# Kernel optimization log

Hardware: AMD Instinct MI355X
Metric: run time of the kernel (lower is better)

## Reference

```python
import jax, jax.numpy as jnp
import numpy as np
import math

HIDDEN = 1024
HEADS = 16
HEAD_DIM = HIDDEN // HEADS
B, S = 2, 2048


def _xavier(key, shape):
    fan_in, fan_out = shape[1], shape[0]
    limit = math.sqrt(6.0 / (fan_in + fan_out))
    return jax.random.uniform(key, shape, jnp.float32, -limit, limit)


def setup_inputs() -> dict:
    key = jax.random.key(0)
    ks = jax.random.split(key, 5)
    x = jax.random.normal(ks[0], (B, S, HIDDEN), jnp.float32)
    # torch Linear stores weight as [out, in]; y = x @ W.T + b
    Wq = _xavier(ks[1], (HIDDEN, HIDDEN))
    Wk = _xavier(ks[2], (HIDDEN, HIDDEN))
    Wv = _xavier(ks[3], (HIDDEN, HIDDEN))
    Wo = _xavier(ks[4], (HIDDEN, HIDDEN))
    bq = jnp.zeros((HIDDEN,), jnp.float32)
    bk = jnp.zeros((HIDDEN,), jnp.float32)
    bv = jnp.zeros((HIDDEN,), jnp.float32)
    bo = jnp.zeros((HIDDEN,), jnp.float32)
    return {"x": x, "Wq": Wq, "bq": bq, "Wk": Wk, "bk": bk,
            "Wv": Wv, "bv": bv, "Wo": Wo, "bo": bo}


def reference(x, Wq, bq, Wk, bk, Wv, bv, Wo, bo):
    b, s, d = x.shape
    h, hd = HEADS, HEAD_DIM
    q = (x @ Wq.T + bq).reshape(b, s, h, hd).transpose(0, 2, 1, 3)  # [b,h,s,hd]
    k = (x @ Wk.T + bk).reshape(b, s, h, hd).transpose(0, 2, 1, 3)
    v = (x @ Wv.T + bv).reshape(b, s, h, hd).transpose(0, 2, 1, 3)
    scores = jnp.einsum('bhqd,bhkd->bhqk', q, k) / math.sqrt(hd)
    causal = jnp.tril(jnp.ones((s, s), bool))
    scores = jnp.where(causal, scores, -jnp.inf)
    attn = jax.nn.softmax(scores, axis=-1)
    out = jnp.einsum('bhqk,bhkd->bhqd', attn, v)  # [b,h,s,hd]
    out = out.transpose(0, 2, 1, 3).reshape(b, s, d)
    return out @ Wo.T + bo
```

## Files before the change

### kernel.cpp

```cpp
#include <hip/hip_runtime.h>
#include <hip/hip_bf16.h>


typedef __hip_bfloat16 bf16;
typedef __attribute__((ext_vector_type(8))) short short8;
typedef __attribute__((ext_vector_type(4))) short short4v;
typedef __attribute__((ext_vector_type(4))) float f32x4;

#define MFMA16(a, b, c) __builtin_amdgcn_mfma_f32_16x16x32_bf16((a), (b), (c), 0, 0, 0)

__device__ __forceinline__ void load_lds16(const void* g, void* l) {
  __builtin_amdgcn_global_load_lds(
      (const __attribute__((address_space(1))) void*)g,
      (__attribute__((address_space(3))) void*)l, 16, 0, 0);
}

#define QSCALE 0.18033688f

__global__ __launch_bounds__(256) void cvt_kernel(
    const float* __restrict__ x, const float* __restrict__ wq,
    const float* __restrict__ wk, const float* __restrict__ wv,
    const float* __restrict__ wo, bf16* __restrict__ xb,
    bf16* __restrict__ wcat) {
  const int bx = blockIdx.x;
  const float* src;
  bf16* dst;
  int ib;
  if (bx < 4096) { src = x; dst = xb; ib = bx; }
  else {
    const int wseg = (bx - 4096) >> 10;
    ib = (bx - 4096) & 1023;
    src = wseg == 0 ? wq : wseg == 1 ? wk : wseg == 2 ? wv : wo;
    dst = wcat + (size_t)wseg * 1048576;
  }
  const int i = (ib * 256 + threadIdx.x) * 4;
  const float4 v = *(const float4*)(src + i);
  short4v p;
  *(__hip_bfloat162*)&p = __float22bfloat162_rn(float2{v.x, v.y});
  *((__hip_bfloat162*)&p + 1) = __float22bfloat162_rn(float2{v.z, v.w});
  *(short4v*)(dst + i) = p;
}

__global__ __launch_bounds__(256) void qkv_kernel(
    const bf16* __restrict__ x, const bf16* __restrict__ Wcat,
    const float* __restrict__ bq, const float* __restrict__ bk,
    const float* __restrict__ bv, bf16* __restrict__ Qb,
    bf16* __restrict__ Kb, bf16* __restrict__ Vtg) {
  constexpr int K = 1024;
  __shared__ bf16 As[128 * 64];
  __shared__ bf16 Bs[128 * 64];
  const int t = threadIdx.x;
  const int lane = t & 63, w = t >> 6;
  const int quad = lane >> 4, r = lane & 15;
  const int m0 = blockIdx.y * 128;
  const int ncol = blockIdx.x * 128;
  const int seg = ncol >> 10;
  const int n0 = ncol & 1023;
  const int wm = w >> 1, wn = w & 1;

  f32x4 acc[4][4] = {};

  for (int k0 = 0; k0 < K; k0 += 64) {
    __syncthreads();
#pragma unroll
    for (int p = 0; p < 4; ++p) {
      const int c = p * 256 + w * 64 + lane;
      const int row = c >> 3;
      const int scb = (c & 7) ^ (row & 7);
      load_lds16(x + (size_t)(m0 + row) * K + k0 + scb * 8, As + c * 8);
    }
#pragma unroll
    for (int p = 0; p < 4; ++p) {
      const int c = p * 256 + w * 64 + lane;
      const int row = c >> 3;
      const int scb = (c & 7) ^ (row & 7);
      load_lds16(Wcat + (size_t)(ncol + row) * K + k0 + scb * 8, Bs + c * 8);
    }
    __syncthreads();
    short8 af[4][2], bfr[4][2];
#pragma unroll
    for (int ks = 0; ks < 2; ++ks) {
#pragma unroll
      for (int i = 0; i < 4; ++i) {
        const int ra = wm * 64 + i * 16 + r;
        af[i][ks] = *(const short8*)(As + ra * 64 +
                                     (((ks * 4 + quad) ^ (ra & 7)) * 8));
        const int rb = wn * 64 + i * 16 + r;
        bfr[i][ks] = *(const short8*)(Bs + rb * 64 +
                                      (((ks * 4 + quad) ^ (rb & 7)) * 8));
      }
    }
#pragma unroll
    for (int ks = 0; ks < 2; ++ks)
#pragma unroll
      for (int i = 0; i < 4; ++i)
#pragma unroll
        for (int j = 0; j < 4; ++j)
          acc[i][j] = MFMA16(af[i][ks], bfr[j][ks], acc[i][j]);
  }

  const float* bias = seg == 0 ? bq : seg == 1 ? bk : bv;
  const float scale = seg == 0 ? QSCALE : 1.0f;
  bf16* dst01 = seg == 0 ? Qb : Kb;
#pragma unroll
  for (int i = 0; i < 4; ++i) {
    const int m = m0 + wm * 64 + i * 16 + quad * 4;
#pragma unroll
    for (int j = 0; j < 4; ++j) {
      const int nn = n0 + wn * 64 + j * 16 + r;
      const float bv_ = bias[nn];
      if (seg == 2) {
        short4v pk;
        *(__hip_bfloat162*)&pk = __float22bfloat162_rn(
            float2{acc[i][j][0] + bv_, acc[i][j][1] + bv_});
        *((__hip_bfloat162*)&pk + 1) = __float22bfloat162_rn(
            float2{acc[i][j][2] + bv_, acc[i][j][3] + bv_});
        *(short4v*)(Vtg + (size_t)nn * 4096 + m) = pk;
      } else {
#pragma unroll
        for (int g = 0; g < 4; ++g)
          dst01[(size_t)(m + g) * 1024 + nn] =
              __float2bfloat16((acc[i][j][g] + bv_) * scale);
      }
    }
  }
}

__global__ __launch_bounds__(256) void proj_kernel(const bf16* __restrict__ X,
                                                   const bf16* __restrict__ W,
                                                   const float* __restrict__ bias,
                                                   float* __restrict__ Y) {
  constexpr int K = 1024, N = 1024;
  __shared__ bf16 As[64 * 64];
  __shared__ bf16 Bs[128 * 64];
  const int t = threadIdx.x;
  const int lane = t & 63, w = t >> 6;
  const int quad = lane >> 4, r = lane & 15;
  const int m0 = blockIdx.y * 64, n0 = blockIdx.x * 128;
  const int wm = w >> 1, wn = w & 1;

  f32x4 acc[2][4] = {};

  for (int k0 = 0; k0 < K; k0 += 64) {
    __syncthreads();
#pragma unroll
    for (int p = 0; p < 2; ++p) {
      const int c = p * 256 + w * 64 + lane;
      const int row = c >> 3;
      const int scb = (c & 7) ^ (row & 7);
      load_lds16(X + (size_t)(m0 + row) * K + k0 + scb * 8, As + c * 8);
    }
#pragma unroll
    for (int p = 0; p < 4; ++p) {
      const int c = p * 256 + w * 64 + lane;
      const int row = c >> 3;
      const int scb = (c & 7) ^ (row & 7);
      load_lds16(W + (size_t)(n0 + row) * K + k0 + scb * 8, Bs + c * 8);
    }
    __syncthreads();
    short8 af[2][2], bfr[4][2];
#pragma unroll
    for (int ks = 0; ks < 2; ++ks) {
#pragma unroll
      for (int i = 0; i < 2; ++i) {
        const int ra = wm * 32 + i * 16 + r;
        af[i][ks] = *(const short8*)(As + ra * 64 +
                                     (((ks * 4 + quad) ^ (ra & 7)) * 8));
      }
#pragma unroll
      for (int j = 0; j < 4; ++j) {
        const int rb = wn * 64 + j * 16 + r;
        bfr[j][ks] = *(const short8*)(Bs + rb * 64 +
                                      (((ks * 4 + quad) ^ (rb & 7)) * 8));
      }
    }
#pragma unroll
    for (int ks = 0; ks < 2; ++ks)
#pragma unroll
      for (int i = 0; i < 2; ++i)
#pragma unroll
        for (int j = 0; j < 4; ++j)
          acc[i][j] = MFMA16(af[i][ks], bfr[j][ks], acc[i][j]);
  }
#pragma unroll
  for (int i = 0; i < 2; ++i) {
    const int m = m0 + wm * 32 + i * 16 + quad * 4;
#pragma unroll
    for (int j = 0; j < 4; ++j) {
      const int n = n0 + wn * 64 + j * 16 + r;
      const float bv = bias[n];
#pragma unroll
      for (int g = 0; g < 4; ++g)
        Y[(size_t)(m + g) * N + n] = acc[i][j][g] + bv;
    }
  }
}

__global__ __launch_bounds__(256, 4) void attn_kernel(const bf16* __restrict__ Qb,
                                                      const bf16* __restrict__ Kb,
                                                      const bf16* __restrict__ Vtg,
                                                      bf16* __restrict__ Ob) {
  const int j = 31 - blockIdx.x;
  const int h = blockIdx.y, b = blockIdx.z;
  const int t = threadIdx.x;
  const int lane = t & 63, w = t >> 6;
  const int quad = lane >> 4, r = lane & 15;

  __shared__ bf16 Ks[2][64 * 64];
  __shared__ bf16 Vt[2][64 * 64];
  __shared__ bf16 Pl[4][16 * 64];

  const int nkt = j + 1;
  const int qrow = j * 64 + w * 16 + r;

  short8 qf[2];
#pragma unroll
  for (int ks = 0; ks < 2; ++ks)
    qf[ks] = *(const short8*)(Qb + (size_t)(b * 2048 + qrow) * 1024 +
                              h * 64 + ks * 32 + quad * 8);

  const bf16 *kg[2], *vg[2];
  int lofs[2];
#pragma unroll
  for (int p = 0; p < 2; ++p) {
    const int c = p * 256 + t;
    const int row = c >> 3, scb = (c & 7) ^ (row & 7);
    kg[p] = Kb + (size_t)(b * 2048 + row) * 1024 + h * 64 + scb * 8;
    vg[p] = Vtg + (size_t)(h * 64 + row) * 4096 + b * 2048 + scb * 8;
    lofs[p] = c * 8;
  }

  auto stage = [&](int kt, int bs) {
#pragma unroll
    for (int p = 0; p < 2; ++p)
      load_lds16(kg[p] + (size_t)kt * 65536, &Ks[bs][lofs[p]]);
#pragma unroll
    for (int p = 0; p < 2; ++p)
      load_lds16(vg[p] + (size_t)kt * 64, &Vt[bs][lofs[p]]);
  };

  f32x4 o[4] = {};
  float lsum = 0.f;
  bf16* const plw = Pl[w];

  auto compute = [&](int kt, int bs, bool mask) {
    const bf16* const ksb = Ks[bs];
    const bf16* const vtb = Vt[bs];
    f32x4 st[4] = {};
#pragma unroll
    for (int ks = 0; ks < 2; ++ks) {
      short8 kf[4];
#pragma unroll
      for (int mt = 0; mt < 4; ++mt) {
        const int key = mt * 16 + r;
        kf[mt] = *(const short8*)(ksb + key * 64 +
                                  (((ks * 4 + quad) ^ (key & 7)) * 8));
      }
#pragma unroll
      for (int mt = 0; mt < 4; ++mt) st[mt] = MFMA16(kf[mt], qf[ks], st[mt]);
    }
    if (mask) {
#pragma unroll
      for (int mt = 0; mt < 4; ++mt)
#pragma unroll
        for (int g = 0; g < 4; ++g) {
          const int key = kt * 64 + mt * 16 + quad * 4 + g;
          if (key > qrow) st[mt][g] = -1e30f;
        }
    }
#pragma unroll
    for (int mt = 0; mt < 4; ++mt) {
      const float p0 = exp2f(st[mt][0]), p1 = exp2f(st[mt][1]);
      const float p2 = exp2f(st[mt][2]), p3 = exp2f(st[mt][3]);
      lsum += (p0 + p1) + (p2 + p3);
      short4v pk;
      *(__hip_bfloat162*)&pk = __float22bfloat162_rn(float2{p0, p1});
      *((__hip_bfloat162*)&pk + 1) = __float22bfloat162_rn(float2{p2, p3});
      const int key8 = mt * 2 + (quad >> 1);
      *(short4v*)(plw + r * 64 + ((key8 ^ (r & 7)) * 8) + (quad & 1) * 4) = pk;
    }
    asm volatile("s_waitcnt lgkmcnt(0)" ::: "memory");
#pragma unroll
    for (int ks = 0; ks < 2; ++ks) {
      short8 vf[4];
#pragma unroll
      for (int mt = 0; mt < 4; ++mt) {
        const int d = mt * 16 + r;
        vf[mt] = *(const short8*)(vtb + d * 64 +
                                  (((ks * 4 + quad) ^ (d & 7)) * 8));
      }
      const short8 pf =
          *(const short8*)(plw + r * 64 + (((ks * 4 + quad) ^ (r & 7)) * 8));
#pragma unroll
      for (int mt = 0; mt < 4; ++mt) o[mt] = MFMA16(vf[mt], pf, o[mt]);
    }
  };

  stage(0, 0);
  int kt = 0;
  for (; kt < nkt - 1; ++kt) {
    stage(kt + 1, (kt + 1) & 1);
    asm volatile("s_waitcnt vmcnt(4)" ::: "memory");
    __builtin_amdgcn_s_barrier();
    __builtin_amdgcn_sched_barrier(0);
    compute(kt, kt & 1, false);
    __builtin_amdgcn_sched_barrier(0);
    __builtin_amdgcn_s_barrier();
  }
  asm volatile("s_waitcnt vmcnt(0)" ::: "memory");
  __builtin_amdgcn_s_barrier();
  __builtin_amdgcn_sched_barrier(0);
  compute(kt, kt & 1, true);

  lsum += __shfl_xor(lsum, 16);
  lsum += __shfl_xor(lsum, 32);
  const float inv = 1.f / lsum;

#pragma unroll
  for (int mt = 0; mt < 4; ++mt) {
    const int d0 = mt * 16 + quad * 4;
    short4v ph;
    *(__hip_bfloat162*)&ph = __float22bfloat162_rn(
        float2{o[mt][0] * inv, o[mt][1] * inv});
    *((__hip_bfloat162*)&ph + 1) = __float22bfloat162_rn(
        float2{o[mt][2] * inv, o[mt][3] * inv});
    *(short4v*)(Ob + (size_t)(b * 2048 + qrow) * 1024 + h * 64 + d0) = ph;
  }
}

extern "C" void kernel_launch(void* const* d_in, const int* in_sizes, int n_in,
                              void* d_out, int out_size, void* d_ws, size_t ws_size,
                              hipStream_t stream) {
  const float* x  = (const float*)d_in[0];
  const float* Wq = (const float*)d_in[1];
  const float* bq = (const float*)d_in[2];
  const float* Wk = (const float*)d_in[3];
  const float* bk = (const float*)d_in[4];
  const float* Wv = (const float*)d_in[5];
  const float* bv = (const float*)d_in[6];
  const float* Wo = (const float*)d_in[7];
  const float* bo = (const float*)d_in[8];
  float* out = (float*)d_out;

  bf16* xb   = (bf16*)d_ws;
  bf16* wcat = xb + (size_t)4096 * 1024;
  bf16* wob  = wcat + (size_t)3 * 1024 * 1024;
  bf16* Qb   = wcat + (size_t)4 * 1024 * 1024;
  bf16* Kb   = Qb  + (size_t)4096 * 1024;
  bf16* Vtg  = Kb  + (size_t)4096 * 1024;
  bf16* Ob   = Vtg + (size_t)4096 * 1024;
  const size_t need = ((size_t)4096 * 1024 * 5 + (size_t)1024 * 1024 * 4) * 2;
  if (ws_size < need) return;

  cvt_kernel<<<8192, 256, 0, stream>>>(x, Wq, Wk, Wv, Wo, xb, wcat);
  qkv_kernel<<<dim3(24, 32), 256, 0, stream>>>(xb, wcat, bq, bk, bv,
                                               Qb, Kb, Vtg);
  attn_kernel<<<dim3(32, 16, 2), 256, 0, stream>>>(Qb, Kb, Vtg, Ob);
  proj_kernel<<<dim3(8, 64), 256, 0, stream>>>(Ob, wob, bo, out);
}
```

Measured before the change: 201.7 us.

## Restructure attention into paired causal passes with split-K warps and permlane P exchange

```diff
diff --git a/kernel.cpp b/kernel.cpp
--- a/kernel.cpp
+++ b/kernel.cpp
@@ -6,6 +6,8 @@
 typedef __attribute__((ext_vector_type(8))) short short8;
 typedef __attribute__((ext_vector_type(4))) short short4v;
 typedef __attribute__((ext_vector_type(4))) float f32x4;
+typedef __attribute__((ext_vector_type(2))) unsigned uint2v;
+typedef __attribute__((ext_vector_type(4))) unsigned uint4v;
 
 #define MFMA16(a, b, c) __builtin_amdgcn_mfma_f32_16x16x32_bf16((a), (b), (c), 0, 0, 0)
 
@@ -196,136 +198,193 @@
   }
 }
 
-__global__ __launch_bounds__(256, 4) void attn_kernel(const bf16* __restrict__ Qb,
+__global__ __launch_bounds__(512, 4) void attn_kernel(const bf16* __restrict__ Qb,
                                                       const bf16* __restrict__ Kb,
                                                       const bf16* __restrict__ Vtg,
                                                       bf16* __restrict__ Ob) {
-  const int j = 31 - blockIdx.x;
-  const int h = blockIdx.y, b = blockIdx.z;
+  const int n = blockIdx.x;
+  const int gl = n & 7, pair = (n >> 3) & 15, gh = n >> 7;
+  const int g = gl + 8 * gh;
+  const int h = g & 15, b = g >> 4;
   const int t = threadIdx.x;
   const int lane = t & 63, w = t >> 6;
+  const int qs = w >> 2, kst = w & 3;
   const int quad = lane >> 4, r = lane & 15;
 
-  __shared__ bf16 Ks[2][64 * 64];
-  __shared__ bf16 Vt[2][64 * 64];
-  __shared__ bf16 Pl[4][16 * 64];
-
-  const int nkt = j + 1;
-  const int qrow = j * 64 + w * 16 + r;
-
-  short8 qf[2];
-#pragma unroll
-  for (int ks = 0; ks < 2; ++ks)
-    qf[ks] = *(const short8*)(Qb + (size_t)(b * 2048 + qrow) * 1024 +
-                              h * 64 + ks * 32 + quad * 8);
-
-  const bf16 *kg[2], *vg[2];
-  int lofs[2];
-#pragma unroll
-  for (int p = 0; p < 2; ++p) {
-    const int c = p * 256 + t;
-    const int row = c >> 3, scb = (c & 7) ^ (row & 7);
-    kg[p] = Kb + (size_t)(b * 2048 + row) * 1024 + h * 64 + scb * 8;
-    vg[p] = Vtg + (size_t)(h * 64 + row) * 4096 + b * 2048 + scb * 8;
-    lofs[p] = c * 8;
-  }
-
-  auto stage = [&](int kt, int bs) {
-#pragma unroll
-    for (int p = 0; p < 2; ++p)
-      load_lds16(kg[p] + (size_t)kt * 65536, &Ks[bs][lofs[p]]);
-#pragma unroll
-    for (int p = 0; p < 2; ++p)
-      load_lds16(vg[p] + (size_t)kt * 64, &Vt[bs][lofs[p]]);
+  __shared__ __align__(16) bf16 smem[32768];
+  bf16* const ks_base = smem;
+  bf16* const vt_base = smem + 16384;
+
+  const int c = t;
+  const int row = c >> 3, scb = (c & 7) ^ (row & 7);
+  const bf16* const kg = Kb + (size_t)(b * 2048 + row) * 1024 + h * 64 + scb * 8;
+  const bf16* const vg = Vtg + (size_t)(h * 64 + row) * 4096 +
+                         (size_t)b * 2048 + scb * 8;
+  const int c8 = c * 8;
+
+  auto stage_tile = [&](int tile, int half, int sub) {
+    load_lds16(kg + (size_t)tile * 65536, ks_base + (half * 2 + sub) * 4096 + c8);
+    load_lds16(vg + tile * 64,            vt_base + (half * 2 + sub) * 4096 + c8);
   };
 
-  f32x4 o[4] = {};
-  float lsum = 0.f;
-  bf16* const plw = Pl[w];
-
-  auto compute = [&](int kt, int bs, bool mask) {
-    const bf16* const ksb = Ks[bs];
-    const bf16* const vtb = Vt[bs];
-    f32x4 st[4] = {};
-#pragma unroll
-    for (int ks = 0; ks < 2; ++ks) {
-      short8 kf[4];
+  auto pass = [&](const int j, const int nt) {
+    const int lt = nt - 1;
+    const int qrow0 = j * 64 + qs * 32 + r;
+
+    short8 qf[2][2];
+#pragma unroll
+    for (int qb = 0; qb < 2; ++qb)
+#pragma unroll
+      for (int ks = 0; ks < 2; ++ks)
+        qf[qb][ks] = *(const short8*)(Qb + (size_t)(b * 2048 + qrow0 + qb * 16) * 1024 +
+                                      h * 64 + ks * 32 + quad * 8);
+
+    f32x4 o[4][2] = {};
+    float lsum[2] = {0.f, 0.f};
+
+    auto do_tile = [&](const bf16* ksb, int ta, unsigned (&cpk)[2][2]) {
+      const int krow = kst * 16 + r;
+      const short8 kf0 = *(const short8*)(ksb + krow * 64 + ((quad ^ (r & 7)) * 8));
+      const short8 kf1 = *(const short8*)(ksb + krow * 64 + (((4 + quad) ^ (r & 7)) * 8));
+      f32x4 st[2] = {};
+#pragma unroll
+      for (int qb = 0; qb < 2; ++qb) {
+        st[qb] = MFMA16(kf0, qf[qb][0], st[qb]);
+        st[qb] = MFMA16(kf1, qf[qb][1], st[qb]);
+      }
+      if (ta == lt) {
+        const int kb = ta * 64 + kst * 16 + quad * 4;
+#pragma unroll
+        for (int qb = 0; qb < 2; ++qb)
+#pragma unroll
+          for (int g4 = 0; g4 < 4; ++g4)
+            if (kb + g4 > qrow0 + qb * 16) st[qb][g4] = -1e30f;
+      }
+#pragma unroll
+      for (int qb = 0; qb < 2; ++qb) {
+        const float p0 = exp2f(st[qb][0]), p1 = exp2f(st[qb][1]);
+        const float p2 = exp2f(st[qb][2]), p3 = exp2f(st[qb][3]);
+        lsum[qb] += (p0 + p1) + (p2 + p3);
+        unsigned u0, u1;
+        *(__hip_bfloat162*)&u0 = __float22bfloat162_rn(float2{p0, p1});
+        *(__hip_bfloat162*)&u1 = __float22bfloat162_rn(float2{p2, p3});
+        cpk[qb][0] = u0;
+        cpk[qb][1] = u1;
+      }
+    };
+
+    stage_tile(0, 0, 0);
+    if (1 < nt) stage_tile(1, 0, 1);
+    const int nsteps = (nt + 1) >> 1;
+    for (int s = 0; s < nsteps; ++s) {
+      const int half = s & 1;
+      const int t2 = 2 * s + 2, t3 = 2 * s + 3;
+      int nn = 0;
+      if (t2 < nt) { stage_tile(t2, half ^ 1, 0); nn += 2; }
+      if (t3 < nt) { stage_tile(t3, half ^ 1, 1); nn += 2; }
+      if (nn == 4)      asm volatile("s_waitcnt vmcnt(4)" ::: "memory");
+      else if (nn == 2) asm volatile("s_waitcnt vmcnt(2)" ::: "memory");
+      else              asm volatile("s_waitcnt vmcnt(0)" ::: "memory");
+      __builtin_amdgcn_s_barrier();
+      __builtin_amdgcn_sched_barrier(0);
+
+      const bool has1 = (2 * s + 1 < nt);
+      unsigned cpk0[2][2], cpk1[2][2];
+      do_tile(ks_base + (half * 2 + 0) * 4096, 2 * s, cpk0);
+      if (has1) do_tile(ks_base + (half * 2 + 1) * 4096, 2 * s + 1, cpk1);
+      else { cpk1[0][0] = cpk1[0][1] = cpk1[1][0] = cpk1[1][1] = 0u; }
+
+      short8 pf[2];
+#pragma unroll
+      for (int qb = 0; qb < 2; ++qb) {
+        unsigned br[4];
+#pragma unroll
+        for (int p = 0; p < 2; ++p) {
+          uint2v s32 = __builtin_amdgcn_permlane32_swap(cpk0[qb][p], cpk1[qb][p],
+                                                        false, false);
+          uint2v s16 = __builtin_amdgcn_permlane16_swap(s32.x, s32.y,
+                                                        false, false);
+          br[p] = s16.x; br[p + 2] = s16.y;
+        }
+        uint4v pv_; pv_.x = br[0]; pv_.y = br[1]; pv_.z = br[2]; pv_.w = br[3];
+        pf[qb] = __builtin_bit_cast(short8, pv_);
+      }
+
+      const bf16* vtb = vt_base + half * 2 * 4096;
+      const int vsub = has1 ? (quad >> 1) * 4096 : 0;
+      const int vslot = ((kst * 2 + (quad & 1)) ^ (r & 7)) * 8;
+      short8 vf[4];
+#pragma unroll
+      for (int mt = 0; mt < 4; ++mt)
+        vf[mt] = *(const short8*)(vtb + vsub + (mt * 16 + r) * 64 + vslot);
+#pragma unroll
+      for (int mt = 0; mt < 4; ++mt)
+#pragma unroll
+        for (int qb = 0; qb < 2; ++qb)
+          o[mt][qb] = MFMA16(vf[mt], pf[qb], o[mt][qb]);
+
+      __builtin_amdgcn_sched_barrier(0);
+      __builtin_amdgcn_s_barrier();
+    }
+
+    __syncthreads();
+    f32x4* const cb = (f32x4*)smem;
+    float* const lsb = (float*)(smem + 24576);
+    if (kst != 0) {
+      const int ki = kst - 1;
+      const int bo = (qs * 3 + ki) * 8 * 64;
+#pragma unroll
+      for (int mt = 0; mt < 4; ++mt)
+#pragma unroll
+        for (int qb = 0; qb < 2; ++qb)
+          cb[bo + (mt * 2 + qb) * 64 + lane] = o[mt][qb];
+      lsb[((qs * 3 + ki) * 2 + 0) * 64 + lane] = lsum[0];
+      lsb[((qs * 3 + ki) * 2 + 1) * 64 + lane] = lsum[1];
+    }
+    __syncthreads();
+    if (kst == 0) {
+#pragma unroll
+      for (int ki = 0; ki < 3; ++ki) {
+        const int bo = (qs * 3 + ki) * 8 * 64;
+#pragma unroll
+        for (int mt = 0; mt < 4; ++mt)
+#pragma unroll
+          for (int qb = 0; qb < 2; ++qb) {
+            const f32x4 a = cb[bo + (mt * 2 + qb) * 64 + lane];
+#pragma unroll
+            for (int g4 = 0; g4 < 4; ++g4) o[mt][qb][g4] += a[g4];
+          }
+        lsum[0] += lsb[((qs * 3 + ki) * 2 + 0) * 64 + lane];
+        lsum[1] += lsb[((qs * 3 + ki) * 2 + 1) * 64 + lane];
+      }
+      float inv[2];
+#pragma unroll
+      for (int qb = 0; qb < 2; ++qb) {
+        float ls = lsum[qb];
+        ls += __shfl_xor(ls, 16);
+        ls += __shfl_xor(ls, 32);
+        inv[qb] = 1.f / ls;
+      }
 #pragma unroll
       for (int mt = 0; mt < 4; ++mt) {
-        const int key = mt * 16 + r;
-        kf[mt] = *(const short8*)(ksb + key * 64 +
-                                  (((ks * 4 + quad) ^ (key & 7)) * 8));
-      }
-#pragma unroll
-      for (int mt = 0; mt < 4; ++mt) st[mt] = MFMA16(kf[mt], qf[ks], st[mt]);
-    }
-    if (mask) {
-#pragma unroll
-      for (int mt = 0; mt < 4; ++mt)
-#pragma unroll
-        for (int g = 0; g < 4; ++g) {
-          const int key = kt * 64 + mt * 16 + quad * 4 + g;
-          if (key > qrow) st[mt][g] = -1e30f;
+        const int d0 = mt * 16 + quad * 4;
+#pragma unroll
+        for (int qb = 0; qb < 2; ++qb) {
+          short4v ph;
+          *(__hip_bfloat162*)&ph = __float22bfloat162_rn(
+              float2{o[mt][qb][0] * inv[qb], o[mt][qb][1] * inv[qb]});
+          *((__hip_bfloat162*)&ph + 1) = __float22bfloat162_rn(
+              float2{o[mt][qb][2] * inv[qb], o[mt][qb][3] * inv[qb]});
+          *(short4v*)(Ob + (size_t)(b * 2048 + qrow0 + qb * 16) * 1024 +
+                      h * 64 + d0) = ph;
         }
-    }
-#pragma unroll
-    for (int mt = 0; mt < 4; ++mt) {
-      const float p0 = exp2f(st[mt][0]), p1 = exp2f(st[mt][1]);
-      const float p2 = exp2f(st[mt][2]), p3 = exp2f(st[mt][3]);
-      lsum += (p0 + p1) + (p2 + p3);
-      short4v pk;
-      *(__hip_bfloat162*)&pk = __float22bfloat162_rn(float2{p0, p1});
-      *((__hip_bfloat162*)&pk + 1) = __float22bfloat162_rn(float2{p2, p3});
-      const int key8 = mt * 2 + (quad >> 1);
-      *(short4v*)(plw + r * 64 + ((key8 ^ (r & 7)) * 8) + (quad & 1) * 4) = pk;
-    }
-    asm volatile("s_waitcnt lgkmcnt(0)" ::: "memory");
-#pragma unroll
-    for (int ks = 0; ks < 2; ++ks) {
-      short8 vf[4];
-#pragma unroll
-      for (int mt = 0; mt < 4; ++mt) {
-        const int d = mt * 16 + r;
-        vf[mt] = *(const short8*)(vtb + d * 64 +
-                                  (((ks * 4 + quad) ^ (d & 7)) * 8));
-      }
-      const short8 pf =
-          *(const short8*)(plw + r * 64 + (((ks * 4 + quad) ^ (r & 7)) * 8));
-#pragma unroll
-      for (int mt = 0; mt < 4; ++mt) o[mt] = MFMA16(vf[mt], pf, o[mt]);
-    }
+      }
+    }
+    __syncthreads();
   };
 
-  stage(0, 0);
-  int kt = 0;
-  for (; kt < nkt - 1; ++kt) {
-    stage(kt + 1, (kt + 1) & 1);
-    asm volatile("s_waitcnt vmcnt(4)" ::: "memory");
-    __builtin_amdgcn_s_barrier();
-    __builtin_amdgcn_sched_barrier(0);
-    compute(kt, kt & 1, false);
-    __builtin_amdgcn_sched_barrier(0);
-    __builtin_amdgcn_s_barrier();
-  }
-  asm volatile("s_waitcnt vmcnt(0)" ::: "memory");
-  __builtin_amdgcn_s_barrier();
-  __builtin_amdgcn_sched_barrier(0);
-  compute(kt, kt & 1, true);
-
-  lsum += __shfl_xor(lsum, 16);
-  lsum += __shfl_xor(lsum, 32);
-  const float inv = 1.f / lsum;
-
-#pragma unroll
-  for (int mt = 0; mt < 4; ++mt) {
-    const int d0 = mt * 16 + quad * 4;
-    short4v ph;
-    *(__hip_bfloat162*)&ph = __float22bfloat162_rn(
-        float2{o[mt][0] * inv, o[mt][1] * inv});
-    *((__hip_bfloat162*)&ph + 1) = __float22bfloat162_rn(
-        float2{o[mt][2] * inv, o[mt][3] * inv});
-    *(short4v*)(Ob + (size_t)(b * 2048 + qrow) * 1024 + h * 64 + d0) = ph;
-  }
+  pass(31 - pair, 32 - pair);
+  pass(pair, pair + 1);
 }
 
 extern "C" void kernel_launch(void* const* d_in, const int* in_sizes, int n_in,
@@ -355,6 +414,6 @@
   cvt_kernel<<<8192, 256, 0, stream>>>(x, Wq, Wk, Wv, Wo, xb, wcat);
   qkv_kernel<<<dim3(24, 32), 256, 0, stream>>>(xb, wcat, bq, bk, bv,
                                                Qb, Kb, Vtg);
-  attn_kernel<<<dim3(32, 16, 2), 256, 0, stream>>>(Qb, Kb, Vtg, Ob);
+  attn_kernel<<<512, 512, 0, stream>>>(Qb, Kb, Vtg, Ob);
   proj_kernel<<<dim3(8, 64), 256, 0, stream>>>(Ob, wob, bo, out);
 }
```

After: 184.9 us. 8.3% less time.

## Rebalance causal attention with paired query tiles and split-key waves

Applied to the files above, without the earlier changes.

```diff
diff --git a/kernel.cpp b/kernel.cpp
--- a/kernel.cpp
+++ b/kernel.cpp
@@ -6,6 +6,8 @@
 typedef __attribute__((ext_vector_type(8))) short short8;
 typedef __attribute__((ext_vector_type(4))) short short4v;
 typedef __attribute__((ext_vector_type(4))) float f32x4;
+typedef __attribute__((ext_vector_type(2))) unsigned uint2v;
+typedef __attribute__((ext_vector_type(4))) unsigned uint4v;
 
 #define MFMA16(a, b, c) __builtin_amdgcn_mfma_f32_16x16x32_bf16((a), (b), (c), 0, 0, 0)
 
@@ -196,136 +198,155 @@
   }
 }
 
-__global__ __launch_bounds__(256, 4) void attn_kernel(const bf16* __restrict__ Qb,
+__global__ __launch_bounds__(512, 8) void attn_kernel(const bf16* __restrict__ Qb,
                                                       const bf16* __restrict__ Kb,
                                                       const bf16* __restrict__ Vtg,
                                                       bf16* __restrict__ Ob) {
-  const int j = 31 - blockIdx.x;
-  const int h = blockIdx.y, b = blockIdx.z;
+  const int n = blockIdx.x;
+  const int gl = n & 7, pair = (n >> 3) & 15, gh = n >> 7;
+  const int g = gl + 8 * gh;
+  const int h = g & 15, b = g >> 4;
   const int t = threadIdx.x;
   const int lane = t & 63, w = t >> 6;
+  const int qs = w >> 1, kst = w & 1;
   const int quad = lane >> 4, r = lane & 15;
 
-  __shared__ bf16 Ks[2][64 * 64];
-  __shared__ bf16 Vt[2][64 * 64];
-  __shared__ bf16 Pl[4][16 * 64];
-
-  const int nkt = j + 1;
-  const int qrow = j * 64 + w * 16 + r;
-
-  short8 qf[2];
-#pragma unroll
-  for (int ks = 0; ks < 2; ++ks)
-    qf[ks] = *(const short8*)(Qb + (size_t)(b * 2048 + qrow) * 1024 +
-                              h * 64 + ks * 32 + quad * 8);
-
-  const bf16 *kg[2], *vg[2];
-  int lofs[2];
-#pragma unroll
-  for (int p = 0; p < 2; ++p) {
-    const int c = p * 256 + t;
-    const int row = c >> 3, scb = (c & 7) ^ (row & 7);
-    kg[p] = Kb + (size_t)(b * 2048 + row) * 1024 + h * 64 + scb * 8;
-    vg[p] = Vtg + (size_t)(h * 64 + row) * 4096 + b * 2048 + scb * 8;
-    lofs[p] = c * 8;
-  }
-
-  auto stage = [&](int kt, int bs) {
-#pragma unroll
-    for (int p = 0; p < 2; ++p)
-      load_lds16(kg[p] + (size_t)kt * 65536, &Ks[bs][lofs[p]]);
-#pragma unroll
-    for (int p = 0; p < 2; ++p)
-      load_lds16(vg[p] + (size_t)kt * 64, &Vt[bs][lofs[p]]);
+  __shared__ __align__(16) bf16 smem[16384];
+  bf16* const ks_base = smem;
+  bf16* const vt_base = smem + 8192;
+
+  const int c = t;
+  const int row = c >> 3, scb = (c & 7) ^ (row & 7);
+  const bf16* const kg = Kb + (size_t)(b * 2048 + row) * 1024 + h * 64 + scb * 8;
+  const bf16* const vg = Vtg + (size_t)(h * 64 + row) * 4096 +
+                         (size_t)b * 2048 + scb * 8;
+  const int c8 = c * 8;
+
+  auto stage_tile = [&](int tile, int buf) {
+    load_lds16(kg + (size_t)tile * 65536, ks_base + buf * 4096 + c8);
+    load_lds16(vg + tile * 64,            vt_base + buf * 4096 + c8);
   };
 
-  f32x4 o[4] = {};
-  float lsum = 0.f;
-  bf16* const plw = Pl[w];
-
-  auto compute = [&](int kt, int bs, bool mask) {
-    const bf16* const ksb = Ks[bs];
-    const bf16* const vtb = Vt[bs];
-    f32x4 st[4] = {};
-#pragma unroll
-    for (int ks = 0; ks < 2; ++ks) {
-      short8 kf[4];
+  auto pass = [&](const int j, const int nt) {
+    const int qrow = j * 64 + qs * 16 + r;
+
+    short8 qf[2];
+#pragma unroll
+    for (int ks = 0; ks < 2; ++ks)
+      qf[ks] = *(const short8*)(Qb + (size_t)(b * 2048 + qrow) * 1024 +
+                                h * 64 + ks * 32 + quad * 8);
+
+    f32x4 o[4] = {};
+    float lsum = 0.f;
+
+    stage_tile(0, 0);
+    for (int s = 0; s < nt; ++s) {
+      if (s + 1 < nt) {
+        stage_tile(s + 1, (s + 1) & 1);
+        asm volatile("s_waitcnt vmcnt(2)" ::: "memory");
+      } else {
+        asm volatile("s_waitcnt vmcnt(0)" ::: "memory");
+      }
+      __builtin_amdgcn_s_barrier();
+      __builtin_amdgcn_sched_barrier(0);
+
+      const bf16* const ksb = ks_base + (s & 1) * 4096;
+      const bf16* const vtb = vt_base + (s & 1) * 4096;
+
+      short8 kf[2][2];
+#pragma unroll
+      for (int mt = 0; mt < 2; ++mt) {
+        const int krow = kst * 32 + mt * 16 + r;
+#pragma unroll
+        for (int ks = 0; ks < 2; ++ks)
+          kf[mt][ks] = *(const short8*)(ksb + krow * 64 +
+                                        (((ks * 4 + quad) ^ (r & 7)) * 8));
+      }
+      f32x4 st[2] = {};
+#pragma unroll
+      for (int mt = 0; mt < 2; ++mt) {
+        st[mt] = MFMA16(kf[mt][0], qf[0], st[mt]);
+        st[mt] = MFMA16(kf[mt][1], qf[1], st[mt]);
+      }
+      if (s == nt - 1) {
+#pragma unroll
+        for (int mt = 0; mt < 2; ++mt) {
+          const int kb = s * 64 + kst * 32 + mt * 16 + quad * 4;
+#pragma unroll
+          for (int g4 = 0; g4 < 4; ++g4)
+            if (kb + g4 > qrow) st[mt][g4] = -1e30f;
+        }
+      }
+      unsigned cpk[2][2];
+#pragma unroll
+      for (int mt = 0; mt < 2; ++mt) {
+        const float p0 = exp2f(st[mt][0]), p1 = exp2f(st[mt][1]);
+        const float p2 = exp2f(st[mt][2]), p3 = exp2f(st[mt][3]);
+        lsum += (p0 + p1) + (p2 + p3);
+        unsigned u0, u1;
+        *(__hip_bfloat162*)&u0 = __float22bfloat162_rn(float2{p0, p1});
+        *(__hip_bfloat162*)&u1 = __float22bfloat162_rn(float2{p2, p3});
+        cpk[mt][0] = u0;
+        cpk[mt][1] = u1;
+      }
+      unsigned br[4];
+#pragma unroll
+      for (int p = 0; p < 2; ++p) {
+        uint2v s32 = __builtin_amdgcn_permlane32_swap(cpk[0][p], cpk[1][p],
+                                                      false, false);
+        uint2v s16 = __builtin_amdgcn_permlane16_swap(s32.x, s32.y,
+                                                      false, false);
+        br[p] = s16.x; br[p + 2] = s16.y;
+      }
+      uint4v pv_; pv_.x = br[0]; pv_.y = br[1]; pv_.z = br[2]; pv_.w = br[3];
+      const short8 pf = __builtin_bit_cast(short8, pv_);
+
 #pragma unroll
       for (int mt = 0; mt < 4; ++mt) {
-        const int key = mt * 16 + r;
-        kf[mt] = *(const short8*)(ksb + key * 64 +
-                                  (((ks * 4 + quad) ^ (key & 7)) * 8));
-      }
-#pragma unroll
-      for (int mt = 0; mt < 4; ++mt) st[mt] = MFMA16(kf[mt], qf[ks], st[mt]);
-    }
-    if (mask) {
-#pragma unroll
-      for (int mt = 0; mt < 4; ++mt)
-#pragma unroll
-        for (int g = 0; g < 4; ++g) {
-          const int key = kt * 64 + mt * 16 + quad * 4 + g;
-          if (key > qrow) st[mt][g] = -1e30f;
-        }
-    }
-#pragma unroll
-    for (int mt = 0; mt < 4; ++mt) {
-      const float p0 = exp2f(st[mt][0]), p1 = exp2f(st[mt][1]);
-      const float p2 = exp2f(st[mt][2]), p3 = exp2f(st[mt][3]);
-      lsum += (p0 + p1) + (p2 + p3);
-      short4v pk;
-      *(__hip_bfloat162*)&pk = __float22bfloat162_rn(float2{p0, p1});
-      *((__hip_bfloat162*)&pk + 1) = __float22bfloat162_rn(float2{p2, p3});
-      const int key8 = mt * 2 + (quad >> 1);
-      *(short4v*)(plw + r * 64 + ((key8 ^ (r & 7)) * 8) + (quad & 1) * 4) = pk;
-    }
-    asm volatile("s_waitcnt lgkmcnt(0)" ::: "memory");
-#pragma unroll
-    for (int ks = 0; ks < 2; ++ks) {
-      short8 vf[4];
+        const short8 vf = *(const short8*)(vtb + (mt * 16 + r) * 64 +
+                                           (((kst * 4 + quad) ^ (r & 7)) * 8));
+        o[mt] = MFMA16(vf, pf, o[mt]);
+      }
+
+      __builtin_amdgcn_sched_barrier(0);
+      __builtin_amdgcn_s_barrier();
+    }
+
+    lsum += __shfl_xor(lsum, 16);
+    lsum += __shfl_xor(lsum, 32);
+    __syncthreads();
+    f32x4* const cb = (f32x4*)smem;
+    float* const lb = (float*)(smem + 8192);
+    if (kst == 1) {
+#pragma unroll
+      for (int mt = 0; mt < 4; ++mt) cb[(qs * 4 + mt) * 64 + lane] = o[mt];
+      lb[qs * 64 + lane] = lsum;
+    }
+    __syncthreads();
+    if (kst == 0) {
 #pragma unroll
       for (int mt = 0; mt < 4; ++mt) {
-        const int d = mt * 16 + r;
-        vf[mt] = *(const short8*)(vtb + d * 64 +
-                                  (((ks * 4 + quad) ^ (d & 7)) * 8));
-      }
-      const short8 pf =
-          *(const short8*)(plw + r * 64 + (((ks * 4 + quad) ^ (r & 7)) * 8));
-#pragma unroll
-      for (int mt = 0; mt < 4; ++mt) o[mt] = MFMA16(vf[mt], pf, o[mt]);
-    }
+        const f32x4 a = cb[(qs * 4 + mt) * 64 + lane];
+#pragma unroll
+        for (int g4 = 0; g4 < 4; ++g4) o[mt][g4] += a[g4];
+      }
+      const float inv = 1.f / (lsum + lb[qs * 64 + lane]);
+#pragma unroll
+      for (int mt = 0; mt < 4; ++mt) {
+        const int d0 = mt * 16 + quad * 4;
+        short4v ph;
+        *(__hip_bfloat162*)&ph = __float22bfloat162_rn(
+            float2{o[mt][0] * inv, o[mt][1] * inv});
+        *((__hip_bfloat162*)&ph + 1) = __float22bfloat162_rn(
+            float2{o[mt][2] * inv, o[mt][3] * inv});
+        *(short4v*)(Ob + (size_t)(b * 2048 + qrow) * 1024 + h * 64 + d0) = ph;
+      }
+    }
+    __syncthreads();
   };
 
-  stage(0, 0);
-  int kt = 0;
-  for (; kt < nkt - 1; ++kt) {
-    stage(kt + 1, (kt + 1) & 1);
-    asm volatile("s_waitcnt vmcnt(4)" ::: "memory");
-    __builtin_amdgcn_s_barrier();
-    __builtin_amdgcn_sched_barrier(0);
-    compute(kt, kt & 1, false);
-    __builtin_amdgcn_sched_barrier(0);
-    __builtin_amdgcn_s_barrier();
-  }
-  asm volatile("s_waitcnt vmcnt(0)" ::: "memory");
-  __builtin_amdgcn_s_barrier();
-  __builtin_amdgcn_sched_barrier(0);
-  compute(kt, kt & 1, true);
-
-  lsum += __shfl_xor(lsum, 16);
-  lsum += __shfl_xor(lsum, 32);
-  const float inv = 1.f / lsum;
-
-#pragma unroll
-  for (int mt = 0; mt < 4; ++mt) {
-    const int d0 = mt * 16 + quad * 4;
-    short4v ph;
-    *(__hip_bfloat162*)&ph = __float22bfloat162_rn(
-        float2{o[mt][0] * inv, o[mt][1] * inv});
-    *((__hip_bfloat162*)&ph + 1) = __float22bfloat162_rn(
-        float2{o[mt][2] * inv, o[mt][3] * inv});
-    *(short4v*)(Ob + (size_t)(b * 2048 + qrow) * 1024 + h * 64 + d0) = ph;
-  }
+  pass(31 - pair, 32 - pair);
+  pass(pair, pair + 1);
 }
 
 extern "C" void kernel_launch(void* const* d_in, const int* in_sizes, int n_in,
@@ -355,6 +376,6 @@
   cvt_kernel<<<8192, 256, 0, stream>>>(x, Wq, Wk, Wv, Wo, xb, wcat);
   qkv_kernel<<<dim3(24, 32), 256, 0, stream>>>(xb, wcat, bq, bk, bv,
                                                Qb, Kb, Vtg);
-  attn_kernel<<<dim3(32, 16, 2), 256, 0, stream>>>(Qb, Kb, Vtg, Ob);
+  attn_kernel<<<512, 512, 0, stream>>>(Qb, Kb, Vtg, Ob);
   proj_kernel<<<dim3(8, 64), 256, 0, stream>>>(Ob, wob, bo, out);
 }
```

New measurement: 184.6 us. 8.5% less time.
